# Kernel optimization log

Measured on AMD Instinct MI355X. Metric: run time of the kernel, lower is better.

Reference implementation:

```python
import jax, jax.numpy as jnp
import numpy as np

H = 2048       # hidden_size
F = 1024       # moe_intermediate_size
E = 32         # n_routed_experts
G = 8          # n_group
TOPK_GROUP = 3
TOP_K = 6      # num_experts_per_tok
N_SHARED = 2
SCALE = 1.0    # routed_scaling_factor
B, S = 1, 2048


def setup_inputs() -> dict:
    key = jax.random.key(0)
    ks = jax.random.split(key, 8)
    std = 0.02
    return {
        "hidden_states": jax.random.normal(ks[0], (B, S, H), dtype=jnp.float32),
        "w_gate": jax.random.normal(ks[1], (E, H), dtype=jnp.float32) * std,
        "wg": jax.random.normal(ks[2], (E, H, F), dtype=jnp.float32) * std,  # stacked gate_proj
        "wu": jax.random.normal(ks[3], (E, H, F), dtype=jnp.float32) * std,  # stacked up_proj
        "wd": jax.random.normal(ks[4], (E, F, H), dtype=jnp.float32) * std,  # stacked down_proj
        "sg": jax.random.normal(ks[5], (N_SHARED * F, H), dtype=jnp.float32) * std,  # shared gate_proj
        "su": jax.random.normal(ks[6], (N_SHARED * F, H), dtype=jnp.float32) * std,  # shared up_proj
        "sd": jax.random.normal(ks[7], (H, N_SHARED * F), dtype=jnp.float32) * std,  # shared down_proj
    }


def reference(hidden_states, w_gate, wg, wu, wd, sg, su, sd):
    b, s, h = hidden_states.shape
    x = hidden_states.reshape(-1, h)                    # [T, H]
    T = x.shape[0]

    # ---- MoEGate (softmax scoring, group_limited_greedy top-k) ----
    logits = x.astype(jnp.float32) @ w_gate.T           # [T, E]
    scores = jax.nn.softmax(logits, axis=-1)
    group_scores = scores.reshape(T, G, E // G).max(axis=-1)          # [T, G]
    _, group_idx = jax.lax.top_k(group_scores, TOPK_GROUP)            # [T, topk_group]
    group_mask = jax.nn.one_hot(group_idx, G, dtype=scores.dtype).sum(axis=1)  # [T, G]
    score_mask = jnp.repeat(group_mask, E // G, axis=-1)              # [T, E]
    tmp_scores = jnp.where(score_mask > 0.5, scores, 0.0)
    topk_weight, topk_idx = jax.lax.top_k(tmp_scores, TOP_K)          # [T, K]
    # norm_topk_prob=True, top_k>1
    topk_weight = topk_weight / (topk_weight.sum(axis=-1, keepdims=True) + 1e-20) * SCALE

    # combine weights per (token, expert): scatter topk weights (indices distinct)
    combine_w = jnp.zeros((T, E), dtype=jnp.float32)
    combine_w = combine_w.at[jnp.arange(T)[:, None], topk_idx].add(topk_weight)

    # ---- routed experts: dense grouped GEMMs, weighted combine ----
    g = jnp.einsum('th,ehf->etf', x, wg)                # [E, T, F]
    u = jnp.einsum('th,ehf->etf', x, wu)                # [E, T, F]
    act = jax.nn.silu(g) * u                            # SiLU gated
    act = act * combine_w.T[:, :, None]                 # fold combine weights before down-proj
    y = jnp.einsum('etf,efh->th', act, wd)              # [T, H]

    # ---- shared experts ----
    shared = (jax.nn.silu(x @ sg.T) * (x @ su.T)) @ sd.T

    return (y + shared).reshape(b, s, h)
```

## Files before the change

kernel.cpp:

```cpp
#include <hip/hip_runtime.h>

#define HD   2048
#define FD   1024
#define NEXP 32
#define TOPK 6
#define TT   2048
#define SDIM 2048
#define NPAIR (TT*TOPK)
#define BSTR 40

typedef __bf16 bf16x8 __attribute__((ext_vector_type(8)));
typedef float  f32x4  __attribute__((ext_vector_type(4)));

#define GLOAD_LDS16(g, l) __builtin_amdgcn_global_load_lds( \
    (const __attribute__((address_space(1))) void*)(g),     \
    (__attribute__((address_space(3))) void*)(l), 16, 0, 0)

__device__ __forceinline__ ushort f2b(float f) {
  __bf16 h = (__bf16)f;
  union { __bf16 h; ushort u; } v; v.h = h;
  return v.u;
}

__device__ __forceinline__ int prow(int r) {
  return (r & ~3) | ((r + (r >> 2)) & 3);
}

__device__ __forceinline__ void argmax32(float &v, int &i) {
  #pragma unroll
  for (int m = 16; m >= 1; m >>= 1) {
    float ov = __shfl_xor(v, m, 32);
    int   oi = __shfl_xor(i, m, 32);
    if (ov > v || (ov == v && oi < i)) { v = ov; i = oi; }
  }
}

__global__ __launch_bounds__(64) void gating_kernel(
    const float* __restrict__ x, const float* __restrict__ wgate,
    int* __restrict__ topk_idx, float* __restrict__ topk_w, int* __restrict__ cnt)
{
  int t = blockIdx.x;
  int l = threadIdx.x;
  int e = l & 31;
  int half = l >> 5;
  const float* xr = x + (size_t)t * HD + half * (HD/2);
  const float* wr = wgate + (size_t)e * HD + half * (HD/2);
  float acc = 0.f;
  for (int i = 0; i < HD/2; i += 4) {
    float4 a = *(const float4*)(xr + i);
    float4 b = *(const float4*)(wr + i);
    acc += a.x*b.x + a.y*b.y + a.z*b.z + a.w*b.w;
  }
  acc += __shfl_xor(acc, 32);
  float logit = acc;
  float mx = logit;
  #pragma unroll
  for (int m = 16; m >= 1; m >>= 1) mx = fmaxf(mx, __shfl_xor(mx, m, 32));
  float p = __expf(logit - mx);
  float s = p;
  #pragma unroll
  for (int m = 16; m >= 1; m >>= 1) s += __shfl_xor(s, m, 32);
  float score = p / s;
  float gs = score;
  gs = fmaxf(gs, __shfl_xor(gs, 1, 32));
  gs = fmaxf(gs, __shfl_xor(gs, 2, 32));
  int g = e >> 2;
  float gw = gs;
  bool ingroup = false;
  for (int r = 0; r < 3; ++r) {
    float v = gw; int gi = g;
    argmax32(v, gi);
    if (g == gi) { ingroup = true; gw = -1.f; }
  }
  float ms = ingroup ? score : 0.f;
  int myrank = -1;
  float denom = 1e-20f;
  float mw = ms;
  for (int r = 0; r < 6; ++r) {
    float v = mw; int ei = e;
    argmax32(v, ei);
    denom += v;
    if (e == ei) { myrank = r; mw = -1.f; }
  }
  if (l < 32 && myrank >= 0) {
    topk_idx[t*TOPK + myrank] = e;
    topk_w  [t*TOPK + myrank] = score / denom;
    atomicAdd(&cnt[e], 1);
  }
}

__global__ void scan_kernel(const int* __restrict__ cnt, int* __restrict__ offs) {
  if (threadIdx.x == 0) {
    int o = 0;
    for (int e = 0; e < NEXP; ++e) { offs[e] = o; o += cnt[e]; }
  }
}

__global__ void fill_kernel(const int* __restrict__ topk_idx, const float* __restrict__ topk_w,
                            const int* __restrict__ offs, int* __restrict__ cur,
                            int* __restrict__ pair_tok, float* __restrict__ pair_w)
{
  int idx = blockIdx.x * blockDim.x + threadIdx.x;
  if (idx >= NPAIR) return;
  int e = topk_idx[idx];
  int p = offs[e] + atomicAdd(&cur[e], 1);
  pair_tok[p] = idx / TOPK;
  pair_w[p]   = topk_w[idx];
}

__global__ void cvt_kernel(const float* __restrict__ x, ushort* __restrict__ xb) {
  int i = blockIdx.x * blockDim.x + threadIdx.x;
  float4 v = ((const float4*)x)[i];
  ((ushort4*)xb)[i] = make_ushort4(f2b(v.x), f2b(v.y), f2b(v.z), f2b(v.w));
}

__global__ __launch_bounds__(256) void gu_routed(
    const ushort* __restrict__ xb, const float* __restrict__ wg, const float* __restrict__ wu,
    const int* __restrict__ pair_tok, const float* __restrict__ pair_w,
    const int* __restrict__ cnt, const int* __restrict__ offs,
    ushort* __restrict__ act)
{
  __shared__ ushort A[2][128*32];
  __shared__ ushort Bg[2][64*BSTR];
  __shared__ ushort Bu[2][64*BSTR];

  int bid = blockIdx.x;
  int wid = (bid & 7) * 1024 + (bid >> 3);
  int mt = wid & 15;
  int nt = (wid >> 4) & 15;
  int e  = wid >> 8;
  int ce = cnt[e];
  int m0 = mt * 128;
  if (m0 >= ce) return;
  int oe = offs[e];
  int n0 = nt * 64;
  int tid = threadIdx.x, lane = tid & 63, w = tid >> 6;

  int csrc = (lane & 3) ^ ((lane >> 3) & 3);
  const ushort* asrc[2];
  #pragma unroll
  for (int j = 0; j < 2; ++j) {
    int r = (2*w + j)*16 + (lane >> 2);
    int pi = min(m0 + r, ce - 1);
    asrc[j] = xb + (size_t)pair_tok[oe + pi] * HD + csrc * 8;
  }
  int tsel = tid >> 7;
  int ttb = tid & 127;
  int fg = ttb & 15, hg = ttb >> 4;
  const float* wsrc = (tsel ? wu : wg) + (size_t)e * HD * FD + (size_t)hg*4*FD + n0 + fg*4;

  int lm = lane & 15, lg = lane >> 4;
  int wr = w >> 1, wc = w & 1;
  int asw = (lm >> 1) & 3;

  f32x4 accg[4][2], accu[4][2];
  #pragma unroll
  for (int m = 0; m < 4; ++m)
    #pragma unroll
    for (int n = 0; n < 2; ++n) { accg[m][n] = f32x4{0,0,0,0}; accu[m][n] = f32x4{0,0,0,0}; }

  float4 rB[4];
  #define GU_ISSUE(T, BUF) do { \
    _Pragma("unroll") \
    for (int j = 0; j < 2; ++j) \
      GLOAD_LDS16(asrc[j] + (T)*32, &A[BUF][(2*w+j)*512]); \
    const float* p = wsrc + (size_t)(T)*32*FD; \
    rB[0] = *(const float4*)(p); \
    rB[1] = *(const float4*)(p + FD); \
    rB[2] = *(const float4*)(p + 2*FD); \
    rB[3] = *(const float4*)(p + 3*FD); \
  } while (0)
  #define GU_WRITE(BUF) do { \
    ushort* dst = tsel ? &Bu[BUF][0] : &Bg[BUF][0]; \
    _Pragma("unroll") \
    for (int c = 0; c < 4; ++c) { \
      int row = fg*4 + ((c + fg) & 3); \
      *(ushort4*)&dst[row*BSTR + hg*4] = \
        make_ushort4(f2b(rB[0][c]), f2b(rB[1][c]), f2b(rB[2][c]), f2b(rB[3][c])); \
    } \
  } while (0)

  GU_ISSUE(0, 0);
  asm volatile("s_waitcnt vmcnt(0)" ::: "memory");
  GU_WRITE(0);
  __syncthreads();

  int cur = 0;
  for (int t = 0; t < HD/32; ++t) {
    if (t + 1 < HD/32) GU_ISSUE(t + 1, cur ^ 1);
    bf16x8 a[4], bg[2], bu[2];
    #pragma unroll
    for (int m = 0; m < 4; ++m)
      a[m] = *(const bf16x8*)&A[cur][(wr*64 + m*16 + lm)*32 + (lg ^ asw)*8];
    #pragma unroll
    for (int n = 0; n < 2; ++n) {
      int row = prow(wc*32 + n*16 + lm);
      bg[n] = *(const bf16x8*)&Bg[cur][row*BSTR + lg*8];
      bu[n] = *(const bf16x8*)&Bu[cur][row*BSTR + lg*8];
    }
    #pragma unroll
    for (int m = 0; m < 4; ++m)
      #pragma unroll
      for (int n = 0; n < 2; ++n) {
        accg[m][n] = __builtin_amdgcn_mfma_f32_16x16x32_bf16(a[m], bg[n], accg[m][n], 0, 0, 0);
        accu[m][n] = __builtin_amdgcn_mfma_f32_16x16x32_bf16(a[m], bu[n], accu[m][n], 0, 0, 0);
      }
    if (t + 1 < HD/32) {
      asm volatile("s_waitcnt vmcnt(0)" ::: "memory");
      GU_WRITE(cur ^ 1);
    }
    __syncthreads();
    cur ^= 1;
  }
  #undef GU_ISSUE
  #undef GU_WRITE

  #pragma unroll
  for (int m = 0; m < 4; ++m) {
    #pragma unroll
    for (int j = 0; j < 4; ++j) {
      int rl = wr*64 + m*16 + lg*4 + j;
      int pi = m0 + rl;
      if (pi >= ce) continue;
      float pwv = pair_w[oe + pi];
      size_t base = (size_t)(oe + pi) * FD + n0 + wc*32;
      #pragma unroll
      for (int n = 0; n < 2; ++n) {
        float gv = accg[m][n][j];
        float uv = accu[m][n][j];
        float sv = gv / (1.f + __expf(-gv));
        act[base + n*16 + lm] = f2b(sv * uv * pwv);
      }
    }
  }
}

__global__ __launch_bounds__(256) void down_routed(
    const ushort* __restrict__ act, const float* __restrict__ wd,
    const int* __restrict__ pair_tok, const int* __restrict__ cnt, const int* __restrict__ offs,
    float* __restrict__ y)
{
  __shared__ ushort A[2][128*32];
  __shared__ ushort Bd[2][128*BSTR];

  int bid = blockIdx.x;
  int wid = (bid & 7) * 1024 + (bid >> 3);
  int mt = wid & 15;
  int nt = (wid >> 4) & 15;
  int e  = wid >> 8;
  int ce = cnt[e];
  int m0 = mt * 128;
  if (m0 >= ce) return;
  int oe = offs[e];
  int n0 = nt * 128;
  int tid = threadIdx.x, lane = tid & 63, w = tid >> 6;

  int csrc = (lane & 3) ^ ((lane >> 3) & 3);
  const ushort* asrc[2];
  #pragma unroll
  for (int j = 0; j < 2; ++j) {
    int r = (2*w + j)*16 + (lane >> 2);
    int pi = min(m0 + r, ce - 1);
    asrc[j] = act + (size_t)(oe + pi) * FD + csrc * 8;
  }
  int fg = tid & 31, hg = tid >> 5;
  const float* wsrc = wd + (size_t)e * FD * HD + (size_t)hg*4*HD + n0 + fg*4;

  int lm = lane & 15, lg = lane >> 4;
  int wr = w >> 1, wc = w & 1;
  int asw = (lm >> 1) & 3;

  f32x4 acc[4][4];
  #pragma unroll
  for (int m = 0; m < 4; ++m)
    #pragma unroll
    for (int n = 0; n < 4; ++n) acc[m][n] = f32x4{0,0,0,0};

  float4 rB[4];
  #define DN_ISSUE(T, BUF) do { \
    _Pragma("unroll") \
    for (int j = 0; j < 2; ++j) \
      GLOAD_LDS16(asrc[j] + (T)*32, &A[BUF][(2*w+j)*512]); \
    const float* p = wsrc + (size_t)(T)*32*HD; \
    rB[0] = *(const float4*)(p); \
    rB[1] = *(const float4*)(p + HD); \
    rB[2] = *(const float4*)(p + 2*HD); \
    rB[3] = *(const float4*)(p + 3*HD); \
  } while (0)
  #define DN_WRITE(BUF) do { \
    _Pragma("unroll") \
    for (int c = 0; c < 4; ++c) { \
      int row = fg*4 + ((c + fg) & 3); \
      *(ushort4*)&Bd[BUF][row*BSTR + hg*4] = \
        make_ushort4(f2b(rB[0][c]), f2b(rB[1][c]), f2b(rB[2][c]), f2b(rB[3][c])); \
    } \
  } while (0)

  DN_ISSUE(0, 0);
  asm volatile("s_waitcnt vmcnt(0)" ::: "memory");
  DN_WRITE(0);
  __syncthreads();

  int cur = 0;
  for (int t = 0; t < FD/32; ++t) {
    if (t + 1 < FD/32) DN_ISSUE(t + 1, cur ^ 1);
    bf16x8 a[4], b[4];
    #pragma unroll
    for (int m = 0; m < 4; ++m)
      a[m] = *(const bf16x8*)&A[cur][(wr*64 + m*16 + lm)*32 + (lg ^ asw)*8];
    #pragma unroll
    for (int n = 0; n < 4; ++n) {
      int row = prow(wc*64 + n*16 + lm);
      b[n] = *(const bf16x8*)&Bd[cur][row*BSTR + lg*8];
    }
    #pragma unroll
    for (int m = 0; m < 4; ++m)
      #pragma unroll
      for (int n = 0; n < 4; ++n)
        acc[m][n] = __builtin_amdgcn_mfma_f32_16x16x32_bf16(a[m], b[n], acc[m][n], 0, 0, 0);
    if (t + 1 < FD/32) {
      asm volatile("s_waitcnt vmcnt(0)" ::: "memory");
      DN_WRITE(cur ^ 1);
    }
    __syncthreads();
    cur ^= 1;
  }
  #undef DN_ISSUE
  #undef DN_WRITE

  #pragma unroll
  for (int m = 0; m < 4; ++m) {
    #pragma unroll
    for (int j = 0; j < 4; ++j) {
      int rl = wr*64 + m*16 + lg*4 + j;
      int pi = m0 + rl;
      if (pi >= ce) continue;
      int tok = pair_tok[oe + pi];
      size_t base = (size_t)tok * HD + n0 + wc*64;
      #pragma unroll
      for (int n = 0; n < 4; ++n)
        atomicAdd(&y[base + n*16 + lm], acc[m][n][j]);
    }
  }
}

__global__ __launch_bounds__(256) void shared_gu(
    const ushort* __restrict__ xb, const float* __restrict__ sg, const float* __restrict__ su,
    ushort* __restrict__ sact)
{
  __shared__ ushort A[2][128*32];
  __shared__ ushort Bg[2][64*BSTR];
  __shared__ ushort Bu[2][64*BSTR];

  int bid = blockIdx.x;
  int wid = (bid & 7) * 64 + (bid >> 3);
  int mt = wid & 15;
  int nt = wid >> 4;
  int m0 = mt * 128;
  int n0 = nt * 64;
  int tid = threadIdx.x, lane = tid & 63, w = tid >> 6;

  int csrc = (lane & 3) ^ ((lane >> 3) & 3);
  const ushort* asrc[2];
  #pragma unroll
  for (int j = 0; j < 2; ++j) {
    int r = (2*w + j)*16 + (lane >> 2);
    asrc[j] = xb + (size_t)(m0 + r) * HD + csrc * 8;
  }
  int tsel = tid >> 7;
  int ttb = tid & 127;
  int bn = ttb >> 1, bsub = ttb & 1;
  const float* bsrc = (tsel ? su : sg) + (size_t)(n0 + bn) * HD + bsub * 16;

  int lm = lane & 15, lg = lane >> 4;
  int wr = w >> 1, wc = w & 1;
  int asw = (lm >> 1) & 3;

  f32x4 accg[4][2], accu[4][2];
  #pragma unroll
  for (int m = 0; m < 4; ++m)
    #pragma unroll
    for (int n = 0; n < 2; ++n) { accg[m][n] = f32x4{0,0,0,0}; accu[m][n] = f32x4{0,0,0,0}; }

  float4 rB[4];
  #define SG_ISSUE(T, BUF) do { \
    _Pragma("unroll") \
    for (int j = 0; j < 2; ++j) \
      GLOAD_LDS16(asrc[j] + (T)*32, &A[BUF][(2*w+j)*512]); \
    const float* p = bsrc + (T)*32; \
    rB[0] = *(const float4*)(p); \
    rB[1] = *(const float4*)(p + 4); \
    rB[2] = *(const float4*)(p + 8); \
    rB[3] = *(const float4*)(p + 12); \
  } while (0)
  #define SG_WRITE(BUF) do { \
    ushort* dst = (tsel ? &Bu[BUF][0] : &Bg[BUF][0]) + bn*BSTR + bsub*16; \
    dst[0]=f2b(rB[0][0]); dst[1]=f2b(rB[0][1]); dst[2]=f2b(rB[0][2]); dst[3]=f2b(rB[0][3]); \
    dst[4]=f2b(rB[1][0]); dst[5]=f2b(rB[1][1]); dst[6]=f2b(rB[1][2]); dst[7]=f2b(rB[1][3]); \
    dst[8]=f2b(rB[2][0]); dst[9]=f2b(rB[2][1]); dst[10]=f2b(rB[2][2]); dst[11]=f2b(rB[2][3]); \
    dst[12]=f2b(rB[3][0]); dst[13]=f2b(rB[3][1]); dst[14]=f2b(rB[3][2]); dst[15]=f2b(rB[3][3]); \
  } while (0)

  SG_ISSUE(0, 0);
  asm volatile("s_waitcnt vmcnt(0)" ::: "memory");
  SG_WRITE(0);
  __syncthreads();

  int cur = 0;
  for (int t = 0; t < HD/32; ++t) {
    if (t + 1 < HD/32) SG_ISSUE(t + 1, cur ^ 1);
    bf16x8 a[4], bg[2], bu[2];
    #pragma unroll
    for (int m = 0; m < 4; ++m)
      a[m] = *(const bf16x8*)&A[cur][(wr*64 + m*16 + lm)*32 + (lg ^ asw)*8];
    #pragma unroll
    for (int n = 0; n < 2; ++n) {
      int row = wc*32 + n*16 + lm;
      bg[n] = *(const bf16x8*)&Bg[cur][row*BSTR + lg*8];
      bu[n] = *(const bf16x8*)&Bu[cur][row*BSTR + lg*8];
    }
    #pragma unroll
    for (int m = 0; m < 4; ++m)
      #pragma unroll
      for (int n = 0; n < 2; ++n) {
        accg[m][n] = __builtin_amdgcn_mfma_f32_16x16x32_bf16(a[m], bg[n], accg[m][n], 0, 0, 0);
        accu[m][n] = __builtin_amdgcn_mfma_f32_16x16x32_bf16(a[m], bu[n], accu[m][n], 0, 0, 0);
      }
    if (t + 1 < HD/32) {
      asm volatile("s_waitcnt vmcnt(0)" ::: "memory");
      SG_WRITE(cur ^ 1);
    }
    __syncthreads();
    cur ^= 1;
  }
  #undef SG_ISSUE
  #undef SG_WRITE

  #pragma unroll
  for (int m = 0; m < 4; ++m) {
    #pragma unroll
    for (int j = 0; j < 4; ++j) {
      int rl = wr*64 + m*16 + lg*4 + j;
      size_t base = (size_t)(m0 + rl) * SDIM + n0 + wc*32;
      #pragma unroll
      for (int n = 0; n < 2; ++n) {
        float gv = accg[m][n][j];
        float uv = accu[m][n][j];
        float sv = gv / (1.f + __expf(-gv));
        sact[base + n*16 + lm] = f2b(sv * uv);
      }
    }
  }
}

__global__ __launch_bounds__(256) void shared_down(
    const ushort* __restrict__ sact, const float* __restrict__ sd, float* __restrict__ y)
{
  __shared__ ushort A[2][128*32];
  __shared__ ushort Bd[2][128*BSTR];

  int bid = blockIdx.x;
  int wid = (bid & 7) * 32 + (bid >> 3);
  int mt = wid & 15;
  int nt = wid >> 4;
  int m0 = mt * 128;
  int n0 = nt * 128;
  int tid = threadIdx.x, lane = tid & 63, w = tid >> 6;

  int csrc = (lane & 3) ^ ((lane >> 3) & 3);
  const ushort* asrc[2];
  #pragma unroll
  for (int j = 0; j < 2; ++j) {
    int r = (2*w + j)*16 + (lane >> 2);
    asrc[j] = sact + (size_t)(m0 + r) * SDIM + csrc * 8;
  }
  int bn = tid >> 1, bsub = tid & 1;
  const float* bsrc = sd + (size_t)(n0 + bn) * SDIM + bsub * 16;

  int lm = lane & 15, lg = lane >> 4;
  int wr = w >> 1, wc = w & 1;
  int asw = (lm >> 1) & 3;

  f32x4 acc[4][4];
  #pragma unroll
  for (int m = 0; m < 4; ++m)
    #pragma unroll
    for (int n = 0; n < 4; ++n) acc[m][n] = f32x4{0,0,0,0};

  float4 rB[4];
  #define SD_ISSUE(T, BUF) do { \
    _Pragma("unroll") \
    for (int j = 0; j < 2; ++j) \
      GLOAD_LDS16(asrc[j] + (T)*32, &A[BUF][(2*w+j)*512]); \
    const float* p = bsrc + (T)*32; \
    rB[0] = *(const float4*)(p); \
    rB[1] = *(const float4*)(p + 4); \
    rB[2] = *(const float4*)(p + 8); \
    rB[3] = *(const float4*)(p + 12); \
  } while (0)
  #define SD_WRITE(BUF) do { \
    ushort* dst = &Bd[BUF][bn*BSTR + bsub*16]; \
    dst[0]=f2b(rB[0][0]); dst[1]=f2b(rB[0][1]); dst[2]=f2b(rB[0][2]); dst[3]=f2b(rB[0][3]); \
    dst[4]=f2b(rB[1][0]); dst[5]=f2b(rB[1][1]); dst[6]=f2b(rB[1][2]); dst[7]=f2b(rB[1][3]); \
    dst[8]=f2b(rB[2][0]); dst[9]=f2b(rB[2][1]); dst[10]=f2b(rB[2][2]); dst[11]=f2b(rB[2][3]); \
    dst[12]=f2b(rB[3][0]); dst[13]=f2b(rB[3][1]); dst[14]=f2b(rB[3][2]); dst[15]=f2b(rB[3][3]); \
  } while (0)

  SD_ISSUE(0, 0);
  asm volatile("s_waitcnt vmcnt(0)" ::: "memory");
  SD_WRITE(0);
  __syncthreads();

  int cur = 0;
  for (int t = 0; t < SDIM/32; ++t) {
    if (t + 1 < SDIM/32) SD_ISSUE(t + 1, cur ^ 1);
    bf16x8 a[4], b[4];
    #pragma unroll
    for (int m = 0; m < 4; ++m)
      a[m] = *(const bf16x8*)&A[cur][(wr*64 + m*16 + lm)*32 + (lg ^ asw)*8];
    #pragma unroll
    for (int n = 0; n < 4; ++n) {
      int row = wc*64 + n*16 + lm;
      b[n] = *(const bf16x8*)&Bd[cur][row*BSTR + lg*8];
    }
    #pragma unroll
    for (int m = 0; m < 4; ++m)
      #pragma unroll
      for (int n = 0; n < 4; ++n)
        acc[m][n] = __builtin_amdgcn_mfma_f32_16x16x32_bf16(a[m], b[n], acc[m][n], 0, 0, 0);
    if (t + 1 < SDIM/32) {
      asm volatile("s_waitcnt vmcnt(0)" ::: "memory");
      SD_WRITE(cur ^ 1);
    }
    __syncthreads();
    cur ^= 1;
  }
  #undef SD_ISSUE
  #undef SD_WRITE

  #pragma unroll
  for (int m = 0; m < 4; ++m) {
    #pragma unroll
    for (int j = 0; j < 4; ++j) {
      int rl = wr*64 + m*16 + lg*4 + j;
      size_t base = (size_t)(m0 + rl) * HD + n0 + wc*64;
      #pragma unroll
      for (int n = 0; n < 4; ++n) {
        size_t idx = base + n*16 + lm;
        y[idx] += acc[m][n][j];
      }
    }
  }
}

extern "C" void kernel_launch(void* const* d_in, const int* in_sizes, int n_in,
                              void* d_out, int out_size, void* d_ws, size_t ws_size,
                              hipStream_t stream) {
  const float* x     = (const float*)d_in[0];
  const float* wgate = (const float*)d_in[1];
  const float* wg    = (const float*)d_in[2];
  const float* wu    = (const float*)d_in[3];
  const float* wd    = (const float*)d_in[4];
  const float* sg    = (const float*)d_in[5];
  const float* su    = (const float*)d_in[6];
  const float* sd    = (const float*)d_in[7];
  float* y = (float*)d_out;
  char* ws = (char*)d_ws;

  ushort* xb   = (ushort*)(ws + 0);
  ushort* act  = (ushort*)(ws + 8388608);
  ushort* sact = (ushort*)(ws + 33554432);
  int*    tidx = (int*)  (ws + 41943040);
  float*  tw   = (float*)(ws + 41992192);
  int*    ptok = (int*)  (ws + 42041344);
  float*  pw   = (float*)(ws + 42090496);
  int*    cnt  = (int*)  (ws + 42139648);
  int*    cur  = (int*)  (ws + 42139776);
  int*    offs = (int*)  (ws + 42139904);

  hipMemsetAsync(cnt, 0, 512, stream);
  hipMemsetAsync(d_out, 0, (size_t)TT * HD * 4, stream);

  cvt_kernel<<<dim3(4096), dim3(256), 0, stream>>>(x, xb);
  gating_kernel<<<dim3(TT), dim3(64), 0, stream>>>(x, wgate, tidx, tw, cnt);
  scan_kernel<<<dim3(1), dim3(64), 0, stream>>>(cnt, offs);
  fill_kernel<<<dim3(48), dim3(256), 0, stream>>>(tidx, tw, offs, cur, ptok, pw);
  gu_routed<<<dim3(8192), dim3(256), 0, stream>>>(xb, wg, wu, ptok, pw, cnt, offs, act);
  down_routed<<<dim3(8192), dim3(256), 0, stream>>>(act, wd, ptok, cnt, offs, y);
  shared_gu<<<dim3(512), dim3(256), 0, stream>>>(xb, sg, su, sact);
  shared_down<<<dim3(256), dim3(256), 0, stream>>>(sact, sd, y);
}
```

Measured before the change: 801.5 us.

## Pre-convert weights to transposed bf16 and run compacted tile-list GEMMs

Adds per-call conversion kernels that turn the fp32 expert and shared weights into K-contiguous bf16 copies in workspace, so the GEMM B operands can be loaded straight into LDS with global_load_lds instead of register loads plus convert. The scan kernel also builds a compact list of non-empty (expert, m-tile) pairs, so the routed grids launch 2048 blocks and skip empty tiles. The MFMA section is raised to high priority with s_setprio. The new path needs a large workspace and adds a full read-and-write pass over all the weights every call; the old fp32 path is kept as a fallback when the workspace is too small.

Measured after the change: 910.3 us. 13.6% more time.

```diff
diff --git a/kernel.cpp b/kernel.cpp
--- a/kernel.cpp
+++ b/kernel.cpp
@@ -8,6 +8,7 @@
 #define SDIM 2048
 #define NPAIR (TT*TOPK)
 #define BSTR 40
+#define TLMAX 128
 
 typedef __bf16 bf16x8 __attribute__((ext_vector_type(8)));
 typedef float  f32x4  __attribute__((ext_vector_type(4)));
@@ -15,6 +16,8 @@
 #define GLOAD_LDS16(g, l) __builtin_amdgcn_global_load_lds( \
     (const __attribute__((address_space(1))) void*)(g),     \
     (__attribute__((address_space(3))) void*)(l), 16, 0, 0)
+
+#define WAIT_VM0  asm volatile("s_waitcnt vmcnt(0)" ::: "memory")
 
 __device__ __forceinline__ ushort f2b(float f) {
   __bf16 h = (__bf16)f;
@@ -89,10 +92,16 @@
   }
 }
 
-__global__ void scan_kernel(const int* __restrict__ cnt, int* __restrict__ offs) {
+__global__ void scan_kernel(const int* __restrict__ cnt, int* __restrict__ offs,
+                            int* __restrict__ tl_e, int* __restrict__ tl_m, int* __restrict__ ntl) {
   if (threadIdx.x == 0) {
-    int o = 0;
-    for (int e = 0; e < NEXP; ++e) { offs[e] = o; o += cnt[e]; }
+    int o = 0, nt = 0;
+    for (int e = 0; e < NEXP; ++e) {
+      offs[e] = o;
+      for (int m = 0; m < cnt[e]; m += 128) { tl_e[nt] = e; tl_m[nt] = m; ++nt; }
+      o += cnt[e];
+    }
+    ntl[0] = nt;
   }
 }
 
@@ -114,7 +123,422 @@
   ((ushort4*)xb)[i] = make_ushort4(f2b(v.x), f2b(v.y), f2b(v.z), f2b(v.w));
 }
 
-__global__ __launch_bounds__(256) void gu_routed(
+__global__ __launch_bounds__(256) void fconv(const float* __restrict__ in, ushort* __restrict__ out) {
+  int i = blockIdx.x * blockDim.x + threadIdx.x;
+  float4 v = ((const float4*)in)[i];
+  ((ushort4*)out)[i] = make_ushort4(f2b(v.x), f2b(v.y), f2b(v.z), f2b(v.w));
+}
+
+#define TSTR 76
+__global__ __launch_bounds__(256) void tconv(const float* __restrict__ in, ushort* __restrict__ out,
+                                             int R, int C) {
+  __shared__ ushort T[64*TSTR];
+  int tiles_c = C >> 6;
+  int bt = blockIdx.x;
+  int r0 = (bt / tiles_c) << 6;
+  int c0 = (bt % tiles_c) << 6;
+  const float* src = in + (size_t)blockIdx.y * R * C;
+  ushort* dst = out + (size_t)blockIdx.y * R * C;
+  int t = threadIdx.x;
+  int row = (t >> 4) << 2;
+  int col4 = (t & 15) << 2;
+  float vv[4][4];
+  #pragma unroll
+  for (int i = 0; i < 4; ++i) {
+    float4 v = *(const float4*)(src + (size_t)(r0 + row + i) * C + c0 + col4);
+    vv[i][0] = v.x; vv[i][1] = v.y; vv[i][2] = v.z; vv[i][3] = v.w;
+  }
+  #pragma unroll
+  for (int cc = 0; cc < 4; ++cc)
+    *(ushort4*)&T[(col4 + cc)*TSTR + row] =
+      make_ushort4(f2b(vv[0][cc]), f2b(vv[1][cc]), f2b(vv[2][cc]), f2b(vv[3][cc]));
+  __syncthreads();
+  int oc = t >> 2;
+  int ok = (t & 3) << 4;
+  ushort4 a0 = *(const ushort4*)&T[oc*TSTR + ok];
+  ushort4 a1 = *(const ushort4*)&T[oc*TSTR + ok + 4];
+  ushort4 a2 = *(const ushort4*)&T[oc*TSTR + ok + 8];
+  ushort4 a3 = *(const ushort4*)&T[oc*TSTR + ok + 12];
+  ushort* d = dst + (size_t)(c0 + oc) * R + r0 + ok;
+  *(ushort4*)(d)     = a0;
+  *(ushort4*)(d + 4) = a1;
+  *(ushort4*)(d + 8) = a2;
+  *(ushort4*)(d + 12) = a3;
+}
+
+
+__global__ __launch_bounds__(256) void gu_routed_b(
+    const ushort* __restrict__ xb, const ushort* __restrict__ wgt, const ushort* __restrict__ wut,
+    const int* __restrict__ pair_tok, const float* __restrict__ pair_w,
+    const int* __restrict__ cnt, const int* __restrict__ offs,
+    const int* __restrict__ tl_e, const int* __restrict__ tl_m, const int* __restrict__ ntl,
+    ushort* __restrict__ act)
+{
+  __shared__ ushort A[2][128*32];
+  __shared__ ushort Bg[2][64*32];
+  __shared__ ushort Bu[2][64*32];
+
+  int bid = blockIdx.x;
+  int wid = (bid & 7) * 256 + (bid >> 3);
+  int tile = wid >> 4;
+  if (tile >= ntl[0]) return;
+  int nt = wid & 15;
+  int e  = tl_e[tile];
+  int m0 = tl_m[tile];
+  int ce = cnt[e];
+  int oe = offs[e];
+  int n0 = nt * 64;
+  int tid = threadIdx.x, lane = tid & 63, w = tid >> 6;
+
+  int csrc = (lane & 3) ^ ((lane >> 3) & 3);
+  const ushort* asrc[2];
+  #pragma unroll
+  for (int j = 0; j < 2; ++j) {
+    int r = (2*w + j)*16 + (lane >> 2);
+    int pi = min(m0 + r, ce - 1);
+    asrc[j] = xb + (size_t)pair_tok[oe + pi] * HD + csrc * 8;
+  }
+  int brow = w*16 + (lane >> 2);
+  const ushort* bgsrc = wgt + ((size_t)e * FD + n0 + brow) * HD + csrc * 8;
+  const ushort* busrc = wut + ((size_t)e * FD + n0 + brow) * HD + csrc * 8;
+
+  int lm = lane & 15, lg = lane >> 4;
+  int wr = w >> 1, wc = w & 1;
+  int asw = (lm >> 1) & 3;
+
+  f32x4 accg[4][2], accu[4][2];
+  #pragma unroll
+  for (int m = 0; m < 4; ++m)
+    #pragma unroll
+    for (int n = 0; n < 2; ++n) { accg[m][n] = f32x4{0,0,0,0}; accu[m][n] = f32x4{0,0,0,0}; }
+
+  #define GUB_ISSUE(T, BUF) do { \
+    GLOAD_LDS16(asrc[0] + (T)*32, &A[BUF][(2*w)*512]); \
+    GLOAD_LDS16(asrc[1] + (T)*32, &A[BUF][(2*w+1)*512]); \
+    GLOAD_LDS16(bgsrc + (T)*32, &Bg[BUF][w*512]); \
+    GLOAD_LDS16(busrc + (T)*32, &Bu[BUF][w*512]); \
+  } while (0)
+
+  GUB_ISSUE(0, 0);
+  WAIT_VM0;
+  __syncthreads();
+  int cur = 0;
+  for (int t = 0; t < 64; ++t) {
+    if (t + 1 < 64) GUB_ISSUE(t + 1, cur ^ 1);
+    bf16x8 a[4], bg[2], bu[2];
+    #pragma unroll
+    for (int m = 0; m < 4; ++m)
+      a[m] = *(const bf16x8*)&A[cur][(wr*64 + m*16 + lm)*32 + (lg ^ asw)*8];
+    #pragma unroll
+    for (int n = 0; n < 2; ++n) {
+      int row = wc*32 + n*16 + lm;
+      bg[n] = *(const bf16x8*)&Bg[cur][row*32 + (lg ^ asw)*8];
+      bu[n] = *(const bf16x8*)&Bu[cur][row*32 + (lg ^ asw)*8];
+    }
+    __builtin_amdgcn_s_setprio(1);
+    #pragma unroll
+    for (int m = 0; m < 4; ++m)
+      #pragma unroll
+      for (int n = 0; n < 2; ++n) {
+        accg[m][n] = __builtin_amdgcn_mfma_f32_16x16x32_bf16(a[m], bg[n], accg[m][n], 0, 0, 0);
+        accu[m][n] = __builtin_amdgcn_mfma_f32_16x16x32_bf16(a[m], bu[n], accu[m][n], 0, 0, 0);
+      }
+    __builtin_amdgcn_s_setprio(0);
+    if (t + 1 < 64) WAIT_VM0;
+    __syncthreads();
+    cur ^= 1;
+  }
+  #undef GUB_ISSUE
+
+  #pragma unroll
+  for (int m = 0; m < 4; ++m) {
+    #pragma unroll
+    for (int j = 0; j < 4; ++j) {
+      int rl = wr*64 + m*16 + lg*4 + j;
+      int pi = m0 + rl;
+      if (pi >= ce) continue;
+      float pwv = pair_w[oe + pi];
+      size_t base = (size_t)(oe + pi) * FD + n0 + wc*32;
+      #pragma unroll
+      for (int n = 0; n < 2; ++n) {
+        float gv = accg[m][n][j];
+        float uv = accu[m][n][j];
+        float sv = gv / (1.f + __expf(-gv));
+        act[base + n*16 + lm] = f2b(sv * uv * pwv);
+      }
+    }
+  }
+}
+
+__global__ __launch_bounds__(256) void down_routed_b(
+    const ushort* __restrict__ act, const ushort* __restrict__ wdt,
+    const int* __restrict__ pair_tok, const int* __restrict__ cnt, const int* __restrict__ offs,
+    const int* __restrict__ tl_e, const int* __restrict__ tl_m, const int* __restrict__ ntl,
+    float* __restrict__ y)
+{
+  __shared__ ushort A[2][128*32];
+  __shared__ ushort Bd[2][128*32];
+
+  int bid = blockIdx.x;
+  int wid = (bid & 7) * 256 + (bid >> 3);
+  int tile = wid >> 4;
+  if (tile >= ntl[0]) return;
+  int nt = wid & 15;
+  int e  = tl_e[tile];
+  int m0 = tl_m[tile];
+  int ce = cnt[e];
+  int oe = offs[e];
+  int n0 = nt * 128;
+  int tid = threadIdx.x, lane = tid & 63, w = tid >> 6;
+
+  int csrc = (lane & 3) ^ ((lane >> 3) & 3);
+  const ushort* asrc[2];
+  const ushort* bsrc[2];
+  #pragma unroll
+  for (int j = 0; j < 2; ++j) {
+    int r = (2*w + j)*16 + (lane >> 2);
+    int pi = min(m0 + r, ce - 1);
+    asrc[j] = act + (size_t)(oe + pi) * FD + csrc * 8;
+    bsrc[j] = wdt + ((size_t)e * HD + n0 + r) * FD + csrc * 8;
+  }
+
+  int lm = lane & 15, lg = lane >> 4;
+  int wr = w >> 1, wc = w & 1;
+  int asw = (lm >> 1) & 3;
+
+  f32x4 acc[4][4];
+  #pragma unroll
+  for (int m = 0; m < 4; ++m)
+    #pragma unroll
+    for (int n = 0; n < 4; ++n) acc[m][n] = f32x4{0,0,0,0};
+
+  #define DNB_ISSUE(T, BUF) do { \
+    GLOAD_LDS16(asrc[0] + (T)*32, &A[BUF][(2*w)*512]); \
+    GLOAD_LDS16(asrc[1] + (T)*32, &A[BUF][(2*w+1)*512]); \
+    GLOAD_LDS16(bsrc[0] + (T)*32, &Bd[BUF][(2*w)*512]); \
+    GLOAD_LDS16(bsrc[1] + (T)*32, &Bd[BUF][(2*w+1)*512]); \
+  } while (0)
+
+  DNB_ISSUE(0, 0);
+  WAIT_VM0;
+  __syncthreads();
+  int cur = 0;
+  for (int t = 0; t < 32; ++t) {
+    if (t + 1 < 32) DNB_ISSUE(t + 1, cur ^ 1);
+    bf16x8 a[4], b[4];
+    #pragma unroll
+    for (int m = 0; m < 4; ++m)
+      a[m] = *(const bf16x8*)&A[cur][(wr*64 + m*16 + lm)*32 + (lg ^ asw)*8];
+    #pragma unroll
+    for (int n = 0; n < 4; ++n) {
+      int row = wc*64 + n*16 + lm;
+      b[n] = *(const bf16x8*)&Bd[cur][row*32 + (lg ^ asw)*8];
+    }
+    __builtin_amdgcn_s_setprio(1);
+    #pragma unroll
+    for (int m = 0; m < 4; ++m)
+      #pragma unroll
+      for (int n = 0; n < 4; ++n)
+        acc[m][n] = __builtin_amdgcn_mfma_f32_16x16x32_bf16(a[m], b[n], acc[m][n], 0, 0, 0);
+    __builtin_amdgcn_s_setprio(0);
+    if (t + 1 < 32) WAIT_VM0;
+    __syncthreads();
+    cur ^= 1;
+  }
+  #undef DNB_ISSUE
+
+  #pragma unroll
+  for (int m = 0; m < 4; ++m) {
+    #pragma unroll
+    for (int j = 0; j < 4; ++j) {
+      int rl = wr*64 + m*16 + lg*4 + j;
+      int pi = m0 + rl;
+      if (pi >= ce) continue;
+      int tok = pair_tok[oe + pi];
+      size_t base = (size_t)tok * HD + n0 + wc*64;
+      #pragma unroll
+      for (int n = 0; n < 4; ++n)
+        atomicAdd(&y[base + n*16 + lm], acc[m][n][j]);
+    }
+  }
+}
+
+__global__ __launch_bounds__(256) void shared_gu_b(
+    const ushort* __restrict__ xb, const ushort* __restrict__ sgb, const ushort* __restrict__ sub,
+    ushort* __restrict__ sact)
+{
+  __shared__ ushort A[2][128*32];
+  __shared__ ushort Bg[2][64*32];
+  __shared__ ushort Bu[2][64*32];
+
+  int bid = blockIdx.x;
+  int wid = (bid & 7) * 64 + (bid >> 3);
+  int mt = wid & 15;
+  int nt = wid >> 4;
+  int m0 = mt * 128;
+  int n0 = nt * 64;
+  int tid = threadIdx.x, lane = tid & 63, w = tid >> 6;
+
+  int csrc = (lane & 3) ^ ((lane >> 3) & 3);
+  const ushort* asrc[2];
+  #pragma unroll
+  for (int j = 0; j < 2; ++j) {
+    int r = (2*w + j)*16 + (lane >> 2);
+    asrc[j] = xb + (size_t)(m0 + r) * HD + csrc * 8;
+  }
+  int brow = w*16 + (lane >> 2);
+  const ushort* bgsrc = sgb + (size_t)(n0 + brow) * HD + csrc * 8;
+  const ushort* busrc = sub + (size_t)(n0 + brow) * HD + csrc * 8;
+
+  int lm = lane & 15, lg = lane >> 4;
+  int wr = w >> 1, wc = w & 1;
+  int asw = (lm >> 1) & 3;
+
+  f32x4 accg[4][2], accu[4][2];
+  #pragma unroll
+  for (int m = 0; m < 4; ++m)
+    #pragma unroll
+    for (int n = 0; n < 2; ++n) { accg[m][n] = f32x4{0,0,0,0}; accu[m][n] = f32x4{0,0,0,0}; }
+
+  #define SGB_ISSUE(T, BUF) do { \
+    GLOAD_LDS16(asrc[0] + (T)*32, &A[BUF][(2*w)*512]); \
+    GLOAD_LDS16(asrc[1] + (T)*32, &A[BUF][(2*w+1)*512]); \
+    GLOAD_LDS16(bgsrc + (T)*32, &Bg[BUF][w*512]); \
+    GLOAD_LDS16(busrc + (T)*32, &Bu[BUF][w*512]); \
+  } while (0)
+
+  SGB_ISSUE(0, 0);
+  WAIT_VM0;
+  __syncthreads();
+  int cur = 0;
+  for (int t = 0; t < 64; ++t) {
+    if (t + 1 < 64) SGB_ISSUE(t + 1, cur ^ 1);
+    bf16x8 a[4], bg[2], bu[2];
+    #pragma unroll
+    for (int m = 0; m < 4; ++m)
+      a[m] = *(const bf16x8*)&A[cur][(wr*64 + m*16 + lm)*32 + (lg ^ asw)*8];
+    #pragma unroll
+    for (int n = 0; n < 2; ++n) {
+      int row = wc*32 + n*16 + lm;
+      bg[n] = *(const bf16x8*)&Bg[cur][row*32 + (lg ^ asw)*8];
+      bu[n] = *(const bf16x8*)&Bu[cur][row*32 + (lg ^ asw)*8];
+    }
+    __builtin_amdgcn_s_setprio(1);
+    #pragma unroll
+    for (int m = 0; m < 4; ++m)
+      #pragma unroll
+      for (int n = 0; n < 2; ++n) {
+        accg[m][n] = __builtin_amdgcn_mfma_f32_16x16x32_bf16(a[m], bg[n], accg[m][n], 0, 0, 0);
+        accu[m][n] = __builtin_amdgcn_mfma_f32_16x16x32_bf16(a[m], bu[n], accu[m][n], 0, 0, 0);
+      }
+    __builtin_amdgcn_s_setprio(0);
+    if (t + 1 < 64) WAIT_VM0;
+    __syncthreads();
+    cur ^= 1;
+  }
+  #undef SGB_ISSUE
+
+  #pragma unroll
+  for (int m = 0; m < 4; ++m) {
+    #pragma unroll
+    for (int j = 0; j < 4; ++j) {
+      int rl = wr*64 + m*16 + lg*4 + j;
+      size_t base = (size_t)(m0 + rl) * SDIM + n0 + wc*32;
+      #pragma unroll
+      for (int n = 0; n < 2; ++n) {
+        float gv = accg[m][n][j];
+        float uv = accu[m][n][j];
+        float sv = gv / (1.f + __expf(-gv));
+        sact[base + n*16 + lm] = f2b(sv * uv);
+      }
+    }
+  }
+}
+
+__global__ __launch_bounds__(256) void shared_down_b(
+    const ushort* __restrict__ sact, const ushort* __restrict__ sdb, float* __restrict__ y)
+{
+  __shared__ ushort A[2][128*32];
+  __shared__ ushort Bd[2][128*32];
+
+  int bid = blockIdx.x;
+  int wid = (bid & 7) * 32 + (bid >> 3);
+  int mt = wid & 15;
+  int nt = wid >> 4;
+  int m0 = mt * 128;
+  int n0 = nt * 128;
+  int tid = threadIdx.x, lane = tid & 63, w = tid >> 6;
+
+  int csrc = (lane & 3) ^ ((lane >> 3) & 3);
+  const ushort* asrc[2];
+  const ushort* bsrc[2];
+  #pragma unroll
+  for (int j = 0; j < 2; ++j) {
+    int r = (2*w + j)*16 + (lane >> 2);
+    asrc[j] = sact + (size_t)(m0 + r) * SDIM + csrc * 8;
+    bsrc[j] = sdb + (size_t)(n0 + r) * SDIM + csrc * 8;
+  }
+
+  int lm = lane & 15, lg = lane >> 4;
+  int wr = w >> 1, wc = w & 1;
+  int asw = (lm >> 1) & 3;
+
+  f32x4 acc[4][4];
+  #pragma unroll
+  for (int m = 0; m < 4; ++m)
+    #pragma unroll
+    for (int n = 0; n < 4; ++n) acc[m][n] = f32x4{0,0,0,0};
+
+  #define SDB_ISSUE(T, BUF) do { \
+    GLOAD_LDS16(asrc[0] + (T)*32, &A[BUF][(2*w)*512]); \
+    GLOAD_LDS16(asrc[1] + (T)*32, &A[BUF][(2*w+1)*512]); \
+    GLOAD_LDS16(bsrc[0] + (T)*32, &Bd[BUF][(2*w)*512]); \
+    GLOAD_LDS16(bsrc[1] + (T)*32, &Bd[BUF][(2*w+1)*512]); \
+  } while (0)
+
+  SDB_ISSUE(0, 0);
+  WAIT_VM0;
+  __syncthreads();
+  int cur = 0;
+  for (int t = 0; t < 64; ++t) {
+    if (t + 1 < 64) SDB_ISSUE(t + 1, cur ^ 1);
+    bf16x8 a[4], b[4];
+    #pragma unroll
+    for (int m = 0; m < 4; ++m)
+      a[m] = *(const bf16x8*)&A[cur][(wr*64 + m*16 + lm)*32 + (lg ^ asw)*8];
+    #pragma unroll
+    for (int n = 0; n < 4; ++n) {
+      int row = wc*64 + n*16 + lm;
+      b[n] = *(const bf16x8*)&Bd[cur][row*32 + (lg ^ asw)*8];
+    }
+    __builtin_amdgcn_s_setprio(1);
+    #pragma unroll
+    for (int m = 0; m < 4; ++m)
+      #pragma unroll
+      for (int n = 0; n < 4; ++n)
+        acc[m][n] = __builtin_amdgcn_mfma_f32_16x16x32_bf16(a[m], b[n], acc[m][n], 0, 0, 0);
+    __builtin_amdgcn_s_setprio(0);
+    if (t + 1 < 64) WAIT_VM0;
+    __syncthreads();
+    cur ^= 1;
+  }
+  #undef SDB_ISSUE
+
+  #pragma unroll
+  for (int m = 0; m < 4; ++m) {
+    #pragma unroll
+    for (int j = 0; j < 4; ++j) {
+      int rl = wr*64 + m*16 + lg*4 + j;
+      size_t base = (size_t)(m0 + rl) * HD + n0 + wc*64;
+      #pragma unroll
+      for (int n = 0; n < 4; ++n)
+        y[base + n*16 + lm] += acc[m][n][j];
+    }
+  }
+}
+
+
+__global__ __launch_bounds__(256) void gu_routed_f(
     const ushort* __restrict__ xb, const float* __restrict__ wg, const float* __restrict__ wu,
     const int* __restrict__ pair_tok, const float* __restrict__ pair_w,
     const int* __restrict__ cnt, const int* __restrict__ offs,
@@ -181,7 +605,7 @@
   } while (0)
 
   GU_ISSUE(0, 0);
-  asm volatile("s_waitcnt vmcnt(0)" ::: "memory");
+  WAIT_VM0;
   GU_WRITE(0);
   __syncthreads();
 
@@ -206,7 +630,7 @@
         accu[m][n] = __builtin_amdgcn_mfma_f32_16x16x32_bf16(a[m], bu[n], accu[m][n], 0, 0, 0);
       }
     if (t + 1 < HD/32) {
-      asm volatile("s_waitcnt vmcnt(0)" ::: "memory");
+      WAIT_VM0;
       GU_WRITE(cur ^ 1);
     }
     __syncthreads();
@@ -235,7 +659,7 @@
   }
 }
 
-__global__ __launch_bounds__(256) void down_routed(
+__global__ __launch_bounds__(256) void down_routed_f(
     const ushort* __restrict__ act, const float* __restrict__ wd,
     const int* __restrict__ pair_tok, const int* __restrict__ cnt, const int* __restrict__ offs,
     float* __restrict__ y)
@@ -297,7 +721,7 @@
   } while (0)
 
   DN_ISSUE(0, 0);
-  asm volatile("s_waitcnt vmcnt(0)" ::: "memory");
+  WAIT_VM0;
   DN_WRITE(0);
   __syncthreads();
 
@@ -319,7 +743,7 @@
       for (int n = 0; n < 4; ++n)
         acc[m][n] = __builtin_amdgcn_mfma_f32_16x16x32_bf16(a[m], b[n], acc[m][n], 0, 0, 0);
     if (t + 1 < FD/32) {
-      asm volatile("s_waitcnt vmcnt(0)" ::: "memory");
+      WAIT_VM0;
       DN_WRITE(cur ^ 1);
     }
     __syncthreads();
@@ -344,7 +768,7 @@
   }
 }
 
-__global__ __launch_bounds__(256) void shared_gu(
+__global__ __launch_bounds__(256) void shared_gu_f(
     const ushort* __restrict__ xb, const float* __restrict__ sg, const float* __restrict__ su,
     ushort* __restrict__ sact)
 {
@@ -402,7 +826,7 @@
   } while (0)
 
   SG_ISSUE(0, 0);
-  asm volatile("s_waitcnt vmcnt(0)" ::: "memory");
+  WAIT_VM0;
   SG_WRITE(0);
   __syncthreads();
 
@@ -427,7 +851,7 @@
         accu[m][n] = __builtin_amdgcn_mfma_f32_16x16x32_bf16(a[m], bu[n], accu[m][n], 0, 0, 0);
       }
     if (t + 1 < HD/32) {
-      asm volatile("s_waitcnt vmcnt(0)" ::: "memory");
+      WAIT_VM0;
       SG_WRITE(cur ^ 1);
     }
     __syncthreads();
@@ -453,7 +877,7 @@
   }
 }
 
-__global__ __launch_bounds__(256) void shared_down(
+__global__ __launch_bounds__(256) void shared_down_f(
     const ushort* __restrict__ sact, const float* __restrict__ sd, float* __restrict__ y)
 {
   __shared__ ushort A[2][128*32];
@@ -507,7 +931,7 @@
   } while (0)
 
   SD_ISSUE(0, 0);
-  asm volatile("s_waitcnt vmcnt(0)" ::: "memory");
+  WAIT_VM0;
   SD_WRITE(0);
   __syncthreads();
 
@@ -529,7 +953,7 @@
       for (int n = 0; n < 4; ++n)
         acc[m][n] = __builtin_amdgcn_mfma_f32_16x16x32_bf16(a[m], b[n], acc[m][n], 0, 0, 0);
     if (t + 1 < SDIM/32) {
-      asm volatile("s_waitcnt vmcnt(0)" ::: "memory");
+      WAIT_VM0;
       SD_WRITE(cur ^ 1);
     }
     __syncthreads();
@@ -545,10 +969,8 @@
       int rl = wr*64 + m*16 + lg*4 + j;
       size_t base = (size_t)(m0 + rl) * HD + n0 + wc*64;
       #pragma unroll
-      for (int n = 0; n < 4; ++n) {
-        size_t idx = base + n*16 + lm;
-        y[idx] += acc[m][n][j];
-      }
+      for (int n = 0; n < 4; ++n)
+        y[base + n*16 + lm] += acc[m][n][j];
     }
   }
 }
@@ -575,18 +997,45 @@
   int*    ptok = (int*)  (ws + 42041344);
   float*  pw   = (float*)(ws + 42090496);
   int*    cnt  = (int*)  (ws + 42139648);
-  int*    cur  = (int*)  (ws + 42139776);
+  int*    curc = (int*)  (ws + 42139776);
   int*    offs = (int*)  (ws + 42139904);
+  int*    tl_e = (int*)  (ws + 42140160);
+  int*    tl_m = (int*)  (ws + 42140672);
+  int*    ntl  = (int*)  (ws + 42141184);
+  ushort* wgt  = (ushort*)(ws + 50331648);
+  ushort* wut  = (ushort*)(ws + 184549376);
+  ushort* wdt  = (ushort*)(ws + 318767104);
+  ushort* sgb  = (ushort*)(ws + 452984832);
+  ushort* sub  = (ushort*)(ws + 461373440);
+  ushort* sdb  = (ushort*)(ws + 469762048);
+  const size_t WS_NEED = 478150656ULL;
 
   hipMemsetAsync(cnt, 0, 512, stream);
   hipMemsetAsync(d_out, 0, (size_t)TT * HD * 4, stream);
 
   cvt_kernel<<<dim3(4096), dim3(256), 0, stream>>>(x, xb);
   gating_kernel<<<dim3(TT), dim3(64), 0, stream>>>(x, wgate, tidx, tw, cnt);
-  scan_kernel<<<dim3(1), dim3(64), 0, stream>>>(cnt, offs);
-  fill_kernel<<<dim3(48), dim3(256), 0, stream>>>(tidx, tw, offs, cur, ptok, pw);
-  gu_routed<<<dim3(8192), dim3(256), 0, stream>>>(xb, wg, wu, ptok, pw, cnt, offs, act);
-  down_routed<<<dim3(8192), dim3(256), 0, stream>>>(act, wd, ptok, cnt, offs, y);
-  shared_gu<<<dim3(512), dim3(256), 0, stream>>>(xb, sg, su, sact);
-  shared_down<<<dim3(256), dim3(256), 0, stream>>>(sact, sd, y);
-}
+  scan_kernel<<<dim3(1), dim3(64), 0, stream>>>(cnt, offs, tl_e, tl_m, ntl);
+  fill_kernel<<<dim3(48), dim3(256), 0, stream>>>(tidx, tw, offs, curc, ptok, pw);
+
+  if (ws_size >= WS_NEED) {
+    tconv<<<dim3(512, NEXP), dim3(256), 0, stream>>>(wg, wgt, HD, FD);
+    tconv<<<dim3(512, NEXP), dim3(256), 0, stream>>>(wu, wut, HD, FD);
+    tconv<<<dim3(512, NEXP), dim3(256), 0, stream>>>(wd, wdt, FD, HD);
+    fconv<<<dim3(4096), dim3(256), 0, stream>>>(sg, sgb);
+    fconv<<<dim3(4096), dim3(256), 0, stream>>>(su, sub);
+    fconv<<<dim3(4096), dim3(256), 0, stream>>>(sd, sdb);
+
+    gu_routed_b<<<dim3(2048), dim3(256), 0, stream>>>(xb, wgt, wut, ptok, pw, cnt, offs,
+                                                      tl_e, tl_m, ntl, act);
+    down_routed_b<<<dim3(2048), dim3(256), 0, stream>>>(act, wdt, ptok, cnt, offs,
+                                                        tl_e, tl_m, ntl, y);
+    shared_gu_b<<<dim3(512), dim3(256), 0, stream>>>(xb, sgb, sub, sact);
+    shared_down_b<<<dim3(256), dim3(256), 0, stream>>>(sact, sdb, y);
+  } else {
+    gu_routed_f<<<dim3(8192), dim3(256), 0, stream>>>(xb, wg, wu, ptok, pw, cnt, offs, act);
+    down_routed_f<<<dim3(8192), dim3(256), 0, stream>>>(act, wd, ptok, cnt, offs, y);
+    shared_gu_f<<<dim3(512), dim3(256), 0, stream>>>(xb, sg, su, sact);
+    shared_down_f<<<dim3(256), dim3(256), 0, stream>>>(sact, sd, y);
+  }
+}
```
